# Optimization experiments

Measured on AMD Instinct MI355X. Metric: run time of the kernel, lower is better.

Reference implementation:

```python
import jax, jax.numpy as jnp
import numpy as np
import math

B, H, N, D = 4, 16, 2048, 64
SCALE = 1.0 / math.sqrt(D)

def setup_inputs() -> dict:
    key = jax.random.key(0)
    kq, kk, kv = jax.random.split(key, 3)
    return {
        "Q": jax.random.normal(kq, (B, H, N, D), dtype=jnp.float32),
        "K": jax.random.normal(kk, (B, H, N, D), dtype=jnp.float32),
        "V": jax.random.normal(kv, (B, H, N, D), dtype=jnp.float32),
    }

def reference(Q, K, V):
    # scores: [B,H,N,N] -- deliberately materialized, matching the torch module
    scores = jnp.einsum("bhnd,bhmd->bhnm", Q, K) * SCALE
    attn = jax.nn.softmax(scores, axis=-1)
    out = jnp.einsum("bhnm,bhmd->bhnd", attn, V)
    return out
```

## Files before the change

### kernel.cpp

```cpp
#include <hip/hip_runtime.h>

#define NSEQ 2048
#define DH 64
#define QSCALE (0.125f * 1.44269504088896340736f)
#define DEFER_THR 11.5415603f
#define QBLK 256
#define KVBLK 64
#define NTILE (NSEQ / KVBLK)
#define KP 72

typedef _Float16 f16x8 __attribute__((ext_vector_type(8)));
typedef _Float16 f16x4 __attribute__((ext_vector_type(4)));
typedef __fp16 fp16x2 __attribute__((ext_vector_type(2)));
typedef float f32x4 __attribute__((ext_vector_type(4)));
typedef unsigned u32x2 __attribute__((ext_vector_type(2)));

#if defined(__has_builtin) && __has_builtin(__builtin_amdgcn_exp2f)
#define EXP2R(x) __builtin_amdgcn_exp2f(x)
#else
static __device__ __forceinline__ float EXP2R(float x) {
    float r; asm("v_exp_f32 %0, %1" : "=v"(r) : "v"(x)); return r;
}
#endif

union TrP { f16x4 h[2]; f16x8 v8; };

#define TRRD(dst, bb, lit) \
    asm volatile("ds_read_b64_tr_b16 %0, %1 offset:" lit : "=v"(dst) : "v"(bb))

#define CVT4(dst, f4) do { \
        union { fp16x2 f2[2]; f16x4 h4; } _u; \
        _u.f2[0] = __builtin_amdgcn_cvt_pkrtz((f4).x, (f4).y); \
        _u.f2[1] = __builtin_amdgcn_cvt_pkrtz((f4).z, (f4).w); \
        (dst) = _u.h4; } while (0)

__global__ __launch_bounds__(512, 4)
void fa_fwd(const float* __restrict__ Qg, const float* __restrict__ Kg,
            const float* __restrict__ Vg, float* __restrict__ Og)
{
    __shared__ _Float16 Kt[2][KVBLK * KP];
    __shared__ _Float16 Vt[2][KVBLK * DH];

    const int tid  = threadIdx.x;
    const int lane = tid & 63;
    const int wv   = tid >> 6;
    const int l15  = lane & 15;
    const int g    = lane >> 4;

    const int id  = blockIdx.x;
    const int w   = (id & 7) * 64 + (id >> 3);
    const int bh  = w >> 3;
    const int qb0 = (w & 7) * QBLK;
    const size_t base = (size_t)bh * NSEQ * DH;

    f16x8 qf[2][2];
#pragma unroll
    for (int u = 0; u < 2; ++u) {
        const float* qp = Qg + base + (size_t)(qb0 + wv * 32 + u * 16 + l15) * DH;
#pragma unroll
        for (int ks = 0; ks < 2; ++ks)
#pragma unroll
            for (int j = 0; j < 8; ++j)
                qf[u][ks][j] = (_Float16)(qp[32 * ks + 8 * g + j] * QSCALE);
    }

    f32x4 acc[2][4];
#pragma unroll
    for (int u = 0; u < 2; ++u)
#pragma unroll
        for (int nt = 0; nt < 4; ++nt)
            acc[u][nt] = (f32x4){0.f, 0.f, 0.f, 0.f};
    float m_run[2] = {-INFINITY, -INFINITY};
    float l_run[2] = {0.f, 0.f};

    const int grp = tid >> 4;
    const int kb4 = grp >> 1;
    const int dh  = (grp & 1) * 32;
    const int kva = kb4 * 4 + (l15 >> 2);
    const int d0a = dh + (l15 & 3) * 4;
    const int d0b = d0a + 16;
    const float* Kbp = Kg + base;
    const float* Vbp = Vg + base;
    const int offA = kva * DH + d0a;
    const int offB = kva * DH + d0b;
    const int vta = ((kva >> 2) * 4 + (d0a >> 4)) * 64 + (kva & 3) * 16 + (d0a & 15);
    const int vtb = ((kva >> 2) * 4 + (d0b >> 4)) * 64 + (kva & 3) * 16 + (d0b & 15);
    const int kta = kva * KP + d0a;
    const int ktb = kva * KP + d0b;

    float4 kra, krb, vra, vrb;
    kra = *(const float4*)(Kbp + offA);
    krb = *(const float4*)(Kbp + offB);
    vra = *(const float4*)(Vbp + offA);
    vrb = *(const float4*)(Vbp + offB);

#define STAGE_WRITE(bb) do { \
        f16x4 h; \
        CVT4(h, kra); *(f16x4*)&Kt[bb][kta] = h; \
        CVT4(h, krb); *(f16x4*)&Kt[bb][ktb] = h; \
        CVT4(h, vra); *(f16x4*)&Vt[bb][vta] = h; \
        CVT4(h, vrb); *(f16x4*)&Vt[bb][vtb] = h; \
    } while (0)

    STAGE_WRITE(0);
    __syncthreads();

    const unsigned vtrb = (unsigned)(size_t)(&Vt[0][0]) + (unsigned)(g * 1024 + l15 * 8);

    for (int t = 0; t < NTILE; ++t) {
        const int c = t & 1;

        if (t + 1 < NTILE) {
            const float* kp = Kbp + (size_t)(t + 1) * KVBLK * DH;
            const float* vp = Vbp + (size_t)(t + 1) * KVBLK * DH;
            kra = *(const float4*)(kp + offA);
            krb = *(const float4*)(kp + offB);
            vra = *(const float4*)(vp + offA);
            vrb = *(const float4*)(vp + offB);
        }

        const unsigned vb  = vtrb + (unsigned)(c * 8192);
        const unsigned b00 = vb;
        const unsigned b01 = vb + 512u;
        const unsigned b10 = vb + 4096u;
        const unsigned b11 = vb + 4608u;

#pragma unroll
        for (int u = 0; u < 2; ++u) {
            f32x4 s[4];
            __builtin_amdgcn_s_setprio(1);
#pragma unroll
            for (int mt = 0; mt < 4; ++mt) {
                const f16x8 k0 = *(const f16x8*)&Kt[c][(l15 + 16 * mt) * KP + 8 * g];
                const f16x8 k1 = *(const f16x8*)&Kt[c][(l15 + 16 * mt) * KP + 32 + 8 * g];
                s[mt] = __builtin_amdgcn_mfma_f32_16x16x32_f16(k0, qf[u][0],
                            (f32x4){0.f, 0.f, 0.f, 0.f}, 0, 0, 0);
                s[mt] = __builtin_amdgcn_mfma_f32_16x16x32_f16(k1, qf[u][1], s[mt], 0, 0, 0);
            }
            __builtin_amdgcn_s_setprio(0);

            float m0 = fmaxf(fmaxf(s[0][0], s[0][1]), s[0][2]);
            float m1 = fmaxf(fmaxf(s[0][3], s[1][0]), s[1][1]);
            float m2 = fmaxf(fmaxf(s[1][2], s[1][3]), s[2][0]);
            float m3 = fmaxf(fmaxf(s[2][1], s[2][2]), s[2][3]);
            float m4 = fmaxf(fmaxf(s[3][0], s[3][1]), s[3][2]);
            float tmax = fmaxf(fmaxf(m0, m1), fmaxf(fmaxf(m2, m3), fmaxf(m4, s[3][3])));
            tmax = fmaxf(tmax, __shfl_xor(tmax, 16));
            tmax = fmaxf(tmax, __shfl_xor(tmax, 32));

            if (!__all(tmax <= m_run[u] + DEFER_THR)) {
                const float m_new = fmaxf(m_run[u], tmax);
                const float fac = EXP2R(m_run[u] - m_new);
                l_run[u] *= fac;
                m_run[u] = m_new;
#pragma unroll
                for (int r = 0; r < 4; ++r) {
                    const float fr = __shfl(fac, 4 * g + r);
#pragma unroll
                    for (int nt = 0; nt < 4; ++nt) acc[u][nt][r] *= fr;
                }
            }

            unsigned W[4][2];
            float psum = 0.f;
#pragma unroll
            for (int mt = 0; mt < 4; ++mt) {
                float p0 = EXP2R(s[mt][0] - m_run[u]);
                float p1 = EXP2R(s[mt][1] - m_run[u]);
                float p2 = EXP2R(s[mt][2] - m_run[u]);
                float p3 = EXP2R(s[mt][3] - m_run[u]);
                psum += (p0 + p1) + (p2 + p3);
                union { fp16x2 f2; unsigned w; } u0, u1;
                u0.f2 = __builtin_amdgcn_cvt_pkrtz(p0, p1);
                u1.f2 = __builtin_amdgcn_cvt_pkrtz(p2, p3);
                W[mt][0] = u0.w;
                W[mt][1] = u1.w;
            }
            psum += __shfl_xor(psum, 16);
            psum += __shfl_xor(psum, 32);
            l_run[u] += psum;

#pragma unroll
            for (int ks = 0; ks < 2; ++ks) {
                unsigned Ta[4];
#pragma unroll
                for (int h = 0; h < 2; ++h) {
                    u32x2 r1 = __builtin_amdgcn_permlane32_swap(W[2 * ks][h], W[2 * ks + 1][h], false, false);
                    u32x2 r2 = __builtin_amdgcn_permlane16_swap(r1[0], r1[1], false, false);
                    Ta[h]     = r2[0];
                    Ta[2 + h] = r2[1];
                }

                TrP tp[4];
                const unsigned bh0 = ks ? b10 : b00;
                const unsigned bh1 = ks ? b11 : b01;
                TRRD(tp[0].h[0], bh0, "0");   TRRD(tp[0].h[1], bh1, "0");
                TRRD(tp[1].h[0], bh0, "128"); TRRD(tp[1].h[1], bh1, "128");
                TRRD(tp[2].h[0], bh0, "256"); TRRD(tp[2].h[1], bh1, "256");
                TRRD(tp[3].h[0], bh0, "384"); TRRD(tp[3].h[1], bh1, "384");
                asm volatile("s_waitcnt lgkmcnt(0)" ::: "memory");
                __builtin_amdgcn_sched_barrier(0);

                union { unsigned w[4]; f16x8 v; } pau;
                pau.w[0] = Ta[0]; pau.w[1] = Ta[1];
                pau.w[2] = Ta[2]; pau.w[3] = Ta[3];

                __builtin_amdgcn_s_setprio(1);
#pragma unroll
                for (int nt = 0; nt < 4; ++nt)
                    acc[u][nt] = __builtin_amdgcn_mfma_f32_16x16x32_f16(pau.v, tp[nt].v8, acc[u][nt], 0, 0, 0);
                __builtin_amdgcn_s_setprio(0);
            }
        }

        if (t + 1 < NTILE) {
            STAGE_WRITE(c ^ 1);
            __syncthreads();
        }
    }

#pragma unroll
    for (int u = 0; u < 2; ++u)
#pragma unroll
        for (int r = 0; r < 4; ++r) {
            const float lr  = __shfl(l_run[u], 4 * g + r);
            const float inv = 1.0f / lr;
            const int row = qb0 + wv * 32 + u * 16 + 4 * g + r;
            float* op = Og + base + (size_t)row * DH;
#pragma unroll
            for (int nt = 0; nt < 4; ++nt)
                op[16 * nt + l15] = acc[u][nt][r] * inv;
        }
}

extern "C" void kernel_launch(void* const* d_in, const int* in_sizes, int n_in,
                              void* d_out, int out_size, void* d_ws, size_t ws_size,
                              hipStream_t stream) {
    const float* Q = (const float*)d_in[0];
    const float* K = (const float*)d_in[1];
    const float* V = (const float*)d_in[2];
    float* O = (float*)d_out;
    fa_fwd<<<dim3(512, 1, 1), dim3(512, 1, 1), 0, stream>>>(Q, K, V, O);
}
```

Baseline: 111.1 us.

## Share K and V LDS fragments across both query sub-blocks per tile

The per-tile loop is restructured so both query sub-blocks (u=0,1) compute their QK^T scores together, reusing each K fragment loaded from LDS. The PV step now loads the transposed V fragments once per k-slice and applies them to both sub-blocks, which halves the LDS reads and lgkmcnt waits for K and V. The cost is more live registers (two score sets and two packed P arrays held at once), which could lower occupancy or cause spills.

After: 101.1 us. -9.0%, faster.

```diff
diff --git a/kernel.cpp b/kernel.cpp
--- a/kernel.cpp
+++ b/kernel.cpp
@@ -125,26 +125,30 @@
         const unsigned b10 = vb + 4096u;
         const unsigned b11 = vb + 4608u;
 
+        f32x4 s[2][4];
+        __builtin_amdgcn_s_setprio(1);
+#pragma unroll
+        for (int mt = 0; mt < 4; ++mt) {
+            const f16x8 k0 = *(const f16x8*)&Kt[c][(l15 + 16 * mt) * KP + 8 * g];
+            const f16x8 k1 = *(const f16x8*)&Kt[c][(l15 + 16 * mt) * KP + 32 + 8 * g];
+            s[0][mt] = __builtin_amdgcn_mfma_f32_16x16x32_f16(k0, qf[0][0],
+                           (f32x4){0.f, 0.f, 0.f, 0.f}, 0, 0, 0);
+            s[0][mt] = __builtin_amdgcn_mfma_f32_16x16x32_f16(k1, qf[0][1], s[0][mt], 0, 0, 0);
+            s[1][mt] = __builtin_amdgcn_mfma_f32_16x16x32_f16(k0, qf[1][0],
+                           (f32x4){0.f, 0.f, 0.f, 0.f}, 0, 0, 0);
+            s[1][mt] = __builtin_amdgcn_mfma_f32_16x16x32_f16(k1, qf[1][1], s[1][mt], 0, 0, 0);
+        }
+        __builtin_amdgcn_s_setprio(0);
+
+        unsigned W[2][4][2];
 #pragma unroll
         for (int u = 0; u < 2; ++u) {
-            f32x4 s[4];
-            __builtin_amdgcn_s_setprio(1);
-#pragma unroll
-            for (int mt = 0; mt < 4; ++mt) {
-                const f16x8 k0 = *(const f16x8*)&Kt[c][(l15 + 16 * mt) * KP + 8 * g];
-                const f16x8 k1 = *(const f16x8*)&Kt[c][(l15 + 16 * mt) * KP + 32 + 8 * g];
-                s[mt] = __builtin_amdgcn_mfma_f32_16x16x32_f16(k0, qf[u][0],
-                            (f32x4){0.f, 0.f, 0.f, 0.f}, 0, 0, 0);
-                s[mt] = __builtin_amdgcn_mfma_f32_16x16x32_f16(k1, qf[u][1], s[mt], 0, 0, 0);
-            }
-            __builtin_amdgcn_s_setprio(0);
-
-            float m0 = fmaxf(fmaxf(s[0][0], s[0][1]), s[0][2]);
-            float m1 = fmaxf(fmaxf(s[0][3], s[1][0]), s[1][1]);
-            float m2 = fmaxf(fmaxf(s[1][2], s[1][3]), s[2][0]);
-            float m3 = fmaxf(fmaxf(s[2][1], s[2][2]), s[2][3]);
-            float m4 = fmaxf(fmaxf(s[3][0], s[3][1]), s[3][2]);
-            float tmax = fmaxf(fmaxf(m0, m1), fmaxf(fmaxf(m2, m3), fmaxf(m4, s[3][3])));
+            float m0 = fmaxf(fmaxf(s[u][0][0], s[u][0][1]), s[u][0][2]);
+            float m1 = fmaxf(fmaxf(s[u][0][3], s[u][1][0]), s[u][1][1]);
+            float m2 = fmaxf(fmaxf(s[u][1][2], s[u][1][3]), s[u][2][0]);
+            float m3 = fmaxf(fmaxf(s[u][2][1], s[u][2][2]), s[u][2][3]);
+            float m4 = fmaxf(fmaxf(s[u][3][0], s[u][3][1]), s[u][3][2]);
+            float tmax = fmaxf(fmaxf(m0, m1), fmaxf(fmaxf(m2, m3), fmaxf(m4, s[u][3][3])));
             tmax = fmaxf(tmax, __shfl_xor(tmax, 16));
             tmax = fmaxf(tmax, __shfl_xor(tmax, 32));
 
@@ -161,46 +165,47 @@
                 }
             }
 
-            unsigned W[4][2];
             float psum = 0.f;
 #pragma unroll
             for (int mt = 0; mt < 4; ++mt) {
-                float p0 = EXP2R(s[mt][0] - m_run[u]);
-                float p1 = EXP2R(s[mt][1] - m_run[u]);
-                float p2 = EXP2R(s[mt][2] - m_run[u]);
-                float p3 = EXP2R(s[mt][3] - m_run[u]);
+                float p0 = EXP2R(s[u][mt][0] - m_run[u]);
+                float p1 = EXP2R(s[u][mt][1] - m_run[u]);
+                float p2 = EXP2R(s[u][mt][2] - m_run[u]);
+                float p3 = EXP2R(s[u][mt][3] - m_run[u]);
                 psum += (p0 + p1) + (p2 + p3);
                 union { fp16x2 f2; unsigned w; } u0, u1;
                 u0.f2 = __builtin_amdgcn_cvt_pkrtz(p0, p1);
                 u1.f2 = __builtin_amdgcn_cvt_pkrtz(p2, p3);
-                W[mt][0] = u0.w;
-                W[mt][1] = u1.w;
+                W[u][mt][0] = u0.w;
+                W[u][mt][1] = u1.w;
             }
             psum += __shfl_xor(psum, 16);
             psum += __shfl_xor(psum, 32);
             l_run[u] += psum;
-
-#pragma unroll
-            for (int ks = 0; ks < 2; ++ks) {
+        }
+
+#pragma unroll
+        for (int ks = 0; ks < 2; ++ks) {
+            TrP tp[4];
+            const unsigned bh0 = ks ? b10 : b00;
+            const unsigned bh1 = ks ? b11 : b01;
+            TRRD(tp[0].h[0], bh0, "0");   TRRD(tp[0].h[1], bh1, "0");
+            TRRD(tp[1].h[0], bh0, "128"); TRRD(tp[1].h[1], bh1, "128");
+            TRRD(tp[2].h[0], bh0, "256"); TRRD(tp[2].h[1], bh1, "256");
+            TRRD(tp[3].h[0], bh0, "384"); TRRD(tp[3].h[1], bh1, "384");
+            asm volatile("s_waitcnt lgkmcnt(0)" ::: "memory");
+            __builtin_amdgcn_sched_barrier(0);
+
+#pragma unroll
+            for (int u = 0; u < 2; ++u) {
                 unsigned Ta[4];
 #pragma unroll
                 for (int h = 0; h < 2; ++h) {
-                    u32x2 r1 = __builtin_amdgcn_permlane32_swap(W[2 * ks][h], W[2 * ks + 1][h], false, false);
+                    u32x2 r1 = __builtin_amdgcn_permlane32_swap(W[u][2 * ks][h], W[u][2 * ks + 1][h], false, false);
                     u32x2 r2 = __builtin_amdgcn_permlane16_swap(r1[0], r1[1], false, false);
                     Ta[h]     = r2[0];
                     Ta[2 + h] = r2[1];
                 }
-
-                TrP tp[4];
-                const unsigned bh0 = ks ? b10 : b00;
-                const unsigned bh1 = ks ? b11 : b01;
-                TRRD(tp[0].h[0], bh0, "0");   TRRD(tp[0].h[1], bh1, "0");
-                TRRD(tp[1].h[0], bh0, "128"); TRRD(tp[1].h[1], bh1, "128");
-                TRRD(tp[2].h[0], bh0, "256"); TRRD(tp[2].h[1], bh1, "256");
-                TRRD(tp[3].h[0], bh0, "384"); TRRD(tp[3].h[1], bh1, "384");
-                asm volatile("s_waitcnt lgkmcnt(0)" ::: "memory");
-                __builtin_amdgcn_sched_barrier(0);
-
                 union { unsigned w[4]; f16x8 v; } pau;
                 pau.w[0] = Ta[0]; pau.w[1] = Ta[1];
                 pau.w[2] = Ta[2]; pau.w[3] = Ta[3];
```
